# Optimization experiments

Measured on AMD Instinct MI355X. Metric: run time of the kernel, lower is better.

The kernel has to match this reference:

```python
import jax, jax.numpy as jnp
import numpy as np

EMBED_DIM = 1024
NUM_HEADS = 16
HEAD_DIM = EMBED_DIM // NUM_HEADS


def setup_inputs() -> dict:
    key = jax.random.key(0)
    ks = jax.random.split(key, 9)
    s = 1.0 / np.sqrt(EMBED_DIM)
    x = jax.random.normal(ks[0], (2, 2048, EMBED_DIM), dtype=jnp.float32)
    Wq = jax.random.uniform(ks[1], (EMBED_DIM, EMBED_DIM), jnp.float32, -s, s)
    bq = jax.random.uniform(ks[2], (EMBED_DIM,), jnp.float32, -s, s)
    Wk = jax.random.uniform(ks[3], (EMBED_DIM, EMBED_DIM), jnp.float32, -s, s)
    bk = jax.random.uniform(ks[4], (EMBED_DIM,), jnp.float32, -s, s)
    Wv = jax.random.uniform(ks[5], (EMBED_DIM, EMBED_DIM), jnp.float32, -s, s)
    bv = jax.random.uniform(ks[6], (EMBED_DIM,), jnp.float32, -s, s)
    Wo = jax.random.uniform(ks[7], (EMBED_DIM, EMBED_DIM), jnp.float32, -s, s)
    bo = jax.random.uniform(ks[8], (EMBED_DIM,), jnp.float32, -s, s)
    return {"x": x, "Wq": Wq, "bq": bq, "Wk": Wk, "bk": bk,
            "Wv": Wv, "bv": bv, "Wo": Wo, "bo": bo}


def reference(x, Wq, bq, Wk, bk, Wv, bv, Wo, bo):
    B, N, C = x.shape
    H, D = NUM_HEADS, HEAD_DIM
    # nn.Linear: y = x @ W.T + b; here W stored as [in, out] so y = x @ W + b
    def split_heads(y):
        return y.reshape(B, N, H, D).transpose(0, 2, 1, 3)  # [B,H,N,D]
    q = split_heads(x @ Wq + bq)
    k = split_heads(x @ Wk + bk)
    v = split_heads(x @ Wv + bv)
    scores = jnp.einsum('bhnd,bhmd->bhnm', q, k) / jnp.sqrt(jnp.float32(D)).astype(x.dtype)
    attn = jax.nn.softmax(scores, axis=-1)
    ctx = jnp.einsum('bhnm,bhmd->bhnd', attn, v)
    ctx = ctx.transpose(0, 2, 1, 3).reshape(B, N, C)
    return ctx @ Wo + bo
```

## Files before the change

kernel.cpp:

```cpp
#include <hip/hip_runtime.h>
#include <hip/hip_bf16.h>
#include <stdint.h>
#include <stddef.h>

using bf16 = __hip_bfloat16;
using bf16x8 = __attribute__((ext_vector_type(8))) short;
using f32x4  = __attribute__((ext_vector_type(4))) float;
using f32x16 = __attribute__((ext_vector_type(16))) float;
typedef unsigned int u32x2 __attribute__((ext_vector_type(2)));
typedef unsigned int u32x4 __attribute__((ext_vector_type(4)));

#define MFMA16(a, b, c) __builtin_amdgcn_mfma_f32_16x16x32_bf16((a), (b), (c), 0, 0, 0)
#define MFMA32(a, b, c) __builtin_amdgcn_mfma_f32_32x32x16_bf16((a), (b), (c), 0, 0, 0)

#define GLD16(g, l)                                                            \
  __builtin_amdgcn_global_load_lds(                                            \
      (const __attribute__((address_space(1))) void*)(g),                      \
      (__attribute__((address_space(3))) void*)(l), 16, 0, 0)

__device__ __forceinline__ float exp2_fast(float x) {
#if __has_builtin(__builtin_amdgcn_exp2f)
  return __builtin_amdgcn_exp2f(x);
#else
  return __expf(x * 0.69314718056f);
#endif
}

__device__ __forceinline__ float fmax3(float a, float b, float c) {
  return fmaxf(fmaxf(a, b), c);
}

__device__ __forceinline__ unsigned int cvtpk_bf16(float lo, float hi) {
  unsigned int r;
  asm("v_cvt_pk_bf16_f32 %0, %1, %2" : "=v"(r) : "v"(lo), "v"(hi));
  return r;
}

__device__ __forceinline__ void permswap(unsigned int& a, unsigned int& b, int hi) {
#if __has_builtin(__builtin_amdgcn_permlane32_swap)
  u32x2 r = __builtin_amdgcn_permlane32_swap(a, b, false, false);
  a = r.x;
  b = r.y;
#else
  unsigned int sa = __shfl_xor((unsigned int)a, 32, 64);
  unsigned int sb = __shfl_xor((unsigned int)b, 32, 64);
  unsigned int an = hi ? sb : a;
  unsigned int bn = hi ? b : sa;
  a = an; b = bn;
#endif
}


__global__ void convert_x(const float* __restrict__ x, bf16* __restrict__ out) {
  const int i = blockIdx.x * 256 + threadIdx.x;
  const float4 v = ((const float4*)x)[i];
  __hip_bfloat162* o2 = (__hip_bfloat162*)(out + (size_t)i * 4);
  o2[0] = __float22bfloat162_rn(make_float2(v.x, v.y));
  o2[1] = __float22bfloat162_rn(make_float2(v.z, v.w));
}

__global__ void convert_w(const float* __restrict__ W0, const float* __restrict__ W1,
                          const float* __restrict__ W2, const float* __restrict__ W3,
                          bf16* __restrict__ Wt) {
  __shared__ float t[32][33];
  const int bx = blockIdx.x;
  const int mat = bx >> 10;
  const float* W = (mat == 0) ? W0 : (mat == 1) ? W1 : (mat == 2) ? W2 : W3;
  const int rem = bx & 1023;
  const int k0 = (rem >> 5) * 32, n0 = (rem & 31) * 32;
  const int c = threadIdx.x & 31, r0 = (threadIdx.x >> 5) * 4;
#pragma unroll
  for (int i = 0; i < 4; ++i) {
    const int r = r0 + i;
    t[r][c] = W[(size_t)(k0 + r) * 1024 + n0 + c];
  }
  __syncthreads();
  bf16* dst = Wt + (size_t)mat * 1024 * 1024;
#pragma unroll
  for (int i = 0; i < 4; ++i) {
    const int rn = r0 + i;
    dst[(size_t)(n0 + rn) * 1024 + k0 + c] = __float2bfloat16(t[c][rn]);
  }
}

__global__ void concat_bias(const float* __restrict__ bq, const float* __restrict__ bk,
                            const float* __restrict__ bv, const float* __restrict__ bo,
                            float* __restrict__ dst) {
  const int i = blockIdx.x * 256 + threadIdx.x;
  const float* src = (i < 1024) ? bq : (i < 2048) ? bk : (i < 3072) ? bv : bo;
  dst[i] = src[i & 1023];
}


template <int MODE>
__global__ __launch_bounds__(256)
void gemm_bt(const bf16* __restrict__ A, const bf16* __restrict__ Bt,
             const float* __restrict__ bias,
             bf16* __restrict__ Qb, bf16* __restrict__ Kb, bf16* __restrict__ Vt,
             float* __restrict__ Of, int K) {
  __shared__ bf16 As[128 * 32];
  __shared__ bf16 Bs[128 * 32];
  const int tid = threadIdx.x;
  const int lane = tid & 63, w = tid >> 6;
  const int wr = w >> 1, wc = w & 1;
  const int lrow = lane & 15, lgk = lane >> 4;
  const int bm = blockIdx.y * 128, bn = blockIdx.x * 128;
  f32x4 acc[4][4] = {};
  const bf16* Ab = A + (size_t)bm * K;
  const bf16* Bb = Bt + (size_t)bn * K;
  const int e0 = tid, e1 = 256 + tid;

  for (int k0 = 0; k0 < K; k0 += 32) {
    GLD16(Ab + (size_t)(e0 >> 2) * K + k0 + (e0 & 3) * 8, As + e0 * 8);
    GLD16(Ab + (size_t)(e1 >> 2) * K + k0 + (e1 & 3) * 8, As + e1 * 8);
    GLD16(Bb + (size_t)(e0 >> 2) * K + k0 + (e0 & 3) * 8, Bs + e0 * 8);
    GLD16(Bb + (size_t)(e1 >> 2) * K + k0 + (e1 & 3) * 8, Bs + e1 * 8);
    asm volatile("s_waitcnt vmcnt(0)" ::: "memory");
    __syncthreads();
    bf16x8 af[4], bfr[4];
#pragma unroll
    for (int m = 0; m < 4; ++m)
      af[m] = *(const bf16x8*)(As + (wr * 64 + m * 16 + lrow) * 32 + lgk * 8);
#pragma unroll
    for (int n = 0; n < 4; ++n)
      bfr[n] = *(const bf16x8*)(Bs + (wc * 64 + n * 16 + lrow) * 32 + lgk * 8);
#pragma unroll
    for (int m = 0; m < 4; ++m)
#pragma unroll
      for (int n = 0; n < 4; ++n)
        acc[m][n] = MFMA16(af[m], bfr[n], acc[m][n]);
    __syncthreads();
  }

  if constexpr (MODE == 0) {
#pragma unroll
    for (int m = 0; m < 4; ++m) {
#pragma unroll
      for (int n = 0; n < 4; ++n) {
        const int col = bn + wc * 64 + n * 16 + lrow;
        const float bv_ = bias[col];
        const int row0 = bm + wr * 64 + m * 16 + lgk * 4;
        const int which = col >> 10;
        const int hd = col & 1023;
        const int h = hd >> 6, d = hd & 63;
        const int b = row0 >> 11, t0 = row0 & 2047;
        const int bh = b * 16 + h;
        if (which == 2) {
          uint2 pk;
          pk.x = cvtpk_bf16(acc[m][n][0] + bv_, acc[m][n][1] + bv_);
          pk.y = cvtpk_bf16(acc[m][n][2] + bv_, acc[m][n][3] + bv_);
          *(uint2*)(Vt + ((size_t)bh * 64 + d) * 2048 + t0) = pk;
        } else if (which == 0) {
#pragma unroll
          for (int j = 0; j < 4; ++j)
            Qb[((size_t)bh * 2048 + t0 + j) * 64 + d] =
                __float2bfloat16((acc[m][n][j] + bv_) * 0.18033688f);
        } else {
#pragma unroll
          for (int j = 0; j < 4; ++j)
            Kb[((size_t)bh * 2048 + t0 + j) * 64 + d] =
                __float2bfloat16(acc[m][n][j] + bv_);
        }
      }
    }
  } else {
#pragma unroll
    for (int m = 0; m < 4; ++m) {
#pragma unroll
      for (int n = 0; n < 4; ++n) {
        const int col = bn + wc * 64 + n * 16 + lrow;
        const float bv_ = bias[col];
        const int row0 = bm + wr * 64 + m * 16 + lgk * 4;
#pragma unroll
        for (int j = 0; j < 4; ++j)
          Of[(size_t)(row0 + j) * 1024 + col] = acc[m][n][j] + bv_;
      }
    }
  }
}

__global__ __launch_bounds__(256, 2)
void attn_kernel(const bf16* __restrict__ Q, const bf16* __restrict__ Kb,
                 const bf16* __restrict__ Vt, bf16* __restrict__ ctx) {
  __shared__ bf16 Kl[2][64 * 64];
  __shared__ bf16 Vl[2][64 * 64];

  const int tid = threadIdx.x, lane = tid & 63, w = tid >> 6;
  const int lo5 = lane & 31, hi = lane >> 5;

  const int bid = blockIdx.x;
  const int xcd = bid & 7, idx = bid >> 3;
  const int bh = (xcd << 2) | (idx >> 4);
  const int qt = idx & 15;
  const int q0 = qt * 128 + w * 32;

  const bf16* Qbh = Q + (size_t)bh * 2048 * 64;
  const bf16* Kbh = Kb + (size_t)bh * 2048 * 64;
  const bf16* Vbh = Vt + (size_t)bh * 64 * 2048;

  bf16x8 qf[4];
#pragma unroll
  for (int f = 0; f < 4; ++f)
    qf[f] = *(const bf16x8*)(Qbh + (size_t)(q0 + lo5) * 64 + f * 16 + hi * 8);

  f32x16 o0 = {}, o1 = {};
  float m2 = -1e30f;
  float lsum = 0.f;

  auto stage = [&](int buf, int kv) {
#pragma unroll
    for (int i = 0; i < 2; ++i) {
      const int c = (w * 2 + i) * 64 + lane;
      const int r = c >> 3, j = c & 7;
      const int js = (j ^ (r & 7)) * 8;
      GLD16(Kbh + (size_t)(kv + r) * 64 + js, &Kl[buf][c * 8]);
      GLD16(Vbh + (size_t)r * 2048 + kv + js, &Vl[buf][c * 8]);
    }
  };

  bf16x8 pa[4];

  auto softmax_pa = [&](f32x16& s0, f32x16& s1) {
    float r1[11];
#pragma unroll
    for (int i = 0; i < 5; ++i)
      r1[i] = fmax3(s0[3 * i], s0[3 * i + 1], s0[3 * i + 2]);
    r1[5] = fmax3(s0[15], s1[0], s1[1]);
#pragma unroll
    for (int i = 0; i < 4; ++i)
      r1[6 + i] = fmax3(s1[2 + 3 * i], s1[3 + 3 * i], s1[4 + 3 * i]);
    r1[10] = fmaxf(s1[14], s1[15]);
    float r2[4];
#pragma unroll
    for (int i = 0; i < 3; ++i) r2[i] = fmax3(r1[3 * i], r1[3 * i + 1], r1[3 * i + 2]);
    r2[3] = fmaxf(r1[9], r1[10]);
    const float pm = fmaxf(fmax3(r2[0], r2[1], r2[2]), r2[3]);
    if (!__all(pm <= m2 + 11.5416f)) {
      const float mx = fmaxf(pm, __shfl_xor(pm, 32, 64));
      const float mn = fmaxf(m2, mx);
      const float corr = exp2_fast(m2 - mn);
      m2 = mn;
      lsum *= corr;
#pragma unroll
      for (int j = 0; j < 16; ++j) { o0[j] *= corr; o1[j] *= corr; }
    }
#pragma unroll
    for (int j = 0; j < 16; ++j) s0[j] = exp2_fast(s0[j] - m2);
#pragma unroll
    for (int j = 0; j < 16; ++j) s1[j] = exp2_fast(s1[j] - m2);
    float a8[8];
#pragma unroll
    for (int j = 0; j < 8; ++j) a8[j] = (s0[j] + s0[j + 8]) + (s1[j] + s1[j + 8]);
    float a4[4];
#pragma unroll
    for (int j = 0; j < 4; ++j) a4[j] = a8[j] + a8[j + 4];
    lsum += (a4[0] + a4[1]) + (a4[2] + a4[3]);
#pragma unroll
    for (int ks = 0; ks < 4; ++ks) {
      const f32x16& s = (ks < 2) ? s0 : s1;
      const int b0 = (ks & 1) * 8;
      unsigned int a0 = cvtpk_bf16(s[b0 + 0], s[b0 + 1]);
      unsigned int c0 = cvtpk_bf16(s[b0 + 4], s[b0 + 5]);
      unsigned int a1 = cvtpk_bf16(s[b0 + 2], s[b0 + 3]);
      unsigned int c1 = cvtpk_bf16(s[b0 + 6], s[b0 + 7]);
      permswap(a0, c0, hi);
      permswap(a1, c1, hi);
      u32x4 tt;
      tt.x = a0; tt.y = a1; tt.z = c0; tt.w = c1;
      pa[ks] = __builtin_bit_cast(bf16x8, tt);
    }
  };

  f32x16 sA0, sA1, sB0, sB1;
  bf16x8 vfA[8], vfB[8];

  auto step = [&](int t, f32x16& sC0, f32x16& sC1, bf16x8 (&vfC)[8],
                  f32x16& sP0, f32x16& sP1, bf16x8 (&vfP)[8]) {
    const int cur = t & 1;
    const int kv = t << 6;
    if (t < 31) stage(cur ^ 1, kv + 64);
    if (t < 31)
      asm volatile("s_waitcnt vmcnt(4)" ::: "memory");
    else
      asm volatile("s_waitcnt vmcnt(0)" ::: "memory");
    __builtin_amdgcn_s_barrier();
    bf16x8 kf[8];
#pragma unroll
    for (int kt = 0; kt < 2; ++kt)
#pragma unroll
      for (int f = 0; f < 4; ++f) {
        const int r = kt * 32 + lo5;
        kf[kt * 4 + f] =
            *(const bf16x8*)(&Kl[cur][(r * 8 + (((f << 1) + hi) ^ (r & 7))) * 8]);
      }
#pragma unroll
    for (int dt = 0; dt < 2; ++dt)
#pragma unroll
      for (int ks = 0; ks < 4; ++ks) {
        const int r = dt * 32 + lo5;
        vfC[dt * 4 + ks] =
            *(const bf16x8*)(&Vl[cur][(r * 8 + (((ks << 1) + hi) ^ (r & 7))) * 8]);
      }
    if (t > 0) softmax_pa(sP0, sP1);
    asm volatile("s_waitcnt lgkmcnt(0)" ::: "memory");
    __builtin_amdgcn_sched_barrier(0);
    __builtin_amdgcn_s_barrier();
    __builtin_amdgcn_s_setprio(1);
    sC0 = f32x16{};
    sC1 = f32x16{};
#pragma unroll
    for (int f = 0; f < 4; ++f) sC0 = MFMA32(kf[f], qf[f], sC0);
#pragma unroll
    for (int f = 0; f < 4; ++f) sC1 = MFMA32(kf[4 + f], qf[f], sC1);
    if (t > 0) {
#pragma unroll
      for (int ks = 0; ks < 4; ++ks) {
        o0 = MFMA32(vfP[ks], pa[ks], o0);
        o1 = MFMA32(vfP[4 + ks], pa[ks], o1);
      }
    }
    __builtin_amdgcn_s_setprio(0);
  };

  stage(0, 0);

  step(0, sA0, sA1, vfA, sB0, sB1, vfB);
  for (int tt = 1; tt < 31; tt += 2) {
    step(tt, sB0, sB1, vfB, sA0, sA1, vfA);
    step(tt + 1, sA0, sA1, vfA, sB0, sB1, vfB);
  }
  step(31, sB0, sB1, vfB, sA0, sA1, vfA);

  softmax_pa(sB0, sB1);
#pragma unroll
  for (int ks = 0; ks < 4; ++ks) {
    o0 = MFMA32(vfB[ks], pa[ks], o0);
    o1 = MFMA32(vfB[4 + ks], pa[ks], o1);
  }

  lsum += __shfl_xor(lsum, 32, 64);
  const float inv = 1.f / lsum;
  const int b = bh >> 4, h = bh & 15;
  bf16* crow = ctx + (size_t)(b * 2048 + q0 + lo5) * 1024 + h * 64;
#pragma unroll
  for (int g = 0; g < 4; ++g) {
    uint2 pk0, pk1;
    pk0.x = cvtpk_bf16(o0[4 * g + 0] * inv, o0[4 * g + 1] * inv);
    pk0.y = cvtpk_bf16(o0[4 * g + 2] * inv, o0[4 * g + 3] * inv);
    pk1.x = cvtpk_bf16(o1[4 * g + 0] * inv, o1[4 * g + 1] * inv);
    pk1.y = cvtpk_bf16(o1[4 * g + 2] * inv, o1[4 * g + 3] * inv);
    *(uint2*)(crow + 8 * g + 4 * hi) = pk0;
    *(uint2*)(crow + 32 + 8 * g + 4 * hi) = pk1;
  }
}


extern "C" void kernel_launch(void* const* d_in, const int* in_sizes, int n_in,
                              void* d_out, int out_size, void* d_ws, size_t ws_size,
                              hipStream_t stream) {
  const float* x  = (const float*)d_in[0];
  const float* Wq = (const float*)d_in[1];
  const float* bq = (const float*)d_in[2];
  const float* Wk = (const float*)d_in[3];
  const float* bk = (const float*)d_in[4];
  const float* Wv = (const float*)d_in[5];
  const float* bv = (const float*)d_in[6];
  const float* Wo = (const float*)d_in[7];
  const float* bo = (const float*)d_in[8];
  float* out = (float*)d_out;

  char* ws = (char*)d_ws;
  bf16* xb  = (bf16*)(ws);
  bf16* Wt  = (bf16*)(ws + ((size_t)8 << 20));
  bf16* Qb  = (bf16*)(ws + ((size_t)16 << 20));
  bf16* Kb  = (bf16*)(ws + ((size_t)24 << 20));
  bf16* Vt  = (bf16*)(ws + ((size_t)32 << 20));
  bf16* ctx = (bf16*)(ws + ((size_t)40 << 20));
  float* ba = (float*)(ws + ((size_t)48 << 20));

  convert_x<<<dim3(4096), dim3(256), 0, stream>>>(x, xb);
  convert_w<<<dim3(4096), dim3(256), 0, stream>>>(Wq, Wk, Wv, Wo, Wt);
  concat_bias<<<dim3(16), dim3(256), 0, stream>>>(bq, bk, bv, bo, ba);

  gemm_bt<0><<<dim3(24, 32), dim3(256), 0, stream>>>(xb, Wt, ba, Qb, Kb, Vt, nullptr, 1024);

  attn_kernel<<<dim3(512), dim3(256), 0, stream>>>(Qb, Kb, Vt, ctx);

  gemm_bt<1><<<dim3(8, 32), dim3(256), 0, stream>>>(
      ctx, Wt + (size_t)3072 * 1024, ba + 3072, nullptr, nullptr, nullptr, out, 1024);
}
```

Baseline: 134.5 us.

## Triple-buffer GEMM and attention LDS loads, split output GEMM into narrower tiles

Both GEMMs now use a three-stage LDS ring with asynchronous global-to-LDS loads issued two tiles ahead, so loads overlap with MFMA work and each iteration needs one barrier instead of two. The attention kernel also moves to a three-deep K/V ring and drops its second barrier and LDS wait per step. The output projection uses 128x64 tiles, doubling the block count so more CUs are busy. In exchange LDS use per block rises, which may lower occupancy, and with fewer barriers there is a risk of overwrite races on the ring buffers.

After: 126.2 us. -6.2%, faster.

```diff
diff --git a/kernel.cpp b/kernel.cpp
--- a/kernel.cpp
+++ b/kernel.cpp
@@ -91,15 +91,13 @@
   dst[i] = src[i & 1023];
 }
 
-
-template <int MODE>
 __global__ __launch_bounds__(256)
-void gemm_bt(const bf16* __restrict__ A, const bf16* __restrict__ Bt,
-             const float* __restrict__ bias,
-             bf16* __restrict__ Qb, bf16* __restrict__ Kb, bf16* __restrict__ Vt,
-             float* __restrict__ Of, int K) {
-  __shared__ bf16 As[128 * 32];
-  __shared__ bf16 Bs[128 * 32];
+void gemm_qkv(const bf16* __restrict__ A, const bf16* __restrict__ Bt,
+              const float* __restrict__ bias,
+              bf16* __restrict__ Qb, bf16* __restrict__ Kb, bf16* __restrict__ Vt,
+              int K) {
+  __shared__ bf16 As[3][128 * 32];
+  __shared__ bf16 Bs[3][128 * 32];
   const int tid = threadIdx.x;
   const int lane = tid & 63, w = tid >> 6;
   const int wr = w >> 1, wc = w & 1;
@@ -109,72 +107,135 @@
   const bf16* Ab = A + (size_t)bm * K;
   const bf16* Bb = Bt + (size_t)bn * K;
   const int e0 = tid, e1 = 256 + tid;
-
-  for (int k0 = 0; k0 < K; k0 += 32) {
-    GLD16(Ab + (size_t)(e0 >> 2) * K + k0 + (e0 & 3) * 8, As + e0 * 8);
-    GLD16(Ab + (size_t)(e1 >> 2) * K + k0 + (e1 & 3) * 8, As + e1 * 8);
-    GLD16(Bb + (size_t)(e0 >> 2) * K + k0 + (e0 & 3) * 8, Bs + e0 * 8);
-    GLD16(Bb + (size_t)(e1 >> 2) * K + k0 + (e1 & 3) * 8, Bs + e1 * 8);
-    asm volatile("s_waitcnt vmcnt(0)" ::: "memory");
-    __syncthreads();
+  const int NT = K >> 5;
+
+  auto stage = [&](int s, int k0) {
+    GLD16(Ab + (size_t)(e0 >> 2) * K + k0 + (e0 & 3) * 8, &As[s][e0 * 8]);
+    GLD16(Ab + (size_t)(e1 >> 2) * K + k0 + (e1 & 3) * 8, &As[s][e1 * 8]);
+    GLD16(Bb + (size_t)(e0 >> 2) * K + k0 + (e0 & 3) * 8, &Bs[s][e0 * 8]);
+    GLD16(Bb + (size_t)(e1 >> 2) * K + k0 + (e1 & 3) * 8, &Bs[s][e1 * 8]);
+  };
+
+  stage(0, 0);
+  stage(1, 32);
+  int cur = 0, nxt = 2;
+  for (int t = 0; t < NT; ++t) {
+    if (t < NT - 1)
+      asm volatile("s_waitcnt vmcnt(4)" ::: "memory");
+    else
+      asm volatile("s_waitcnt vmcnt(0)" ::: "memory");
+    __builtin_amdgcn_s_barrier();
+    if (t + 2 < NT) {
+      stage(nxt, (t + 2) << 5);
+      nxt = (nxt == 2) ? 0 : nxt + 1;
+    }
     bf16x8 af[4], bfr[4];
 #pragma unroll
     for (int m = 0; m < 4; ++m)
-      af[m] = *(const bf16x8*)(As + (wr * 64 + m * 16 + lrow) * 32 + lgk * 8);
+      af[m] = *(const bf16x8*)(&As[cur][(wr * 64 + m * 16 + lrow) * 32 + lgk * 8]);
 #pragma unroll
     for (int n = 0; n < 4; ++n)
-      bfr[n] = *(const bf16x8*)(Bs + (wc * 64 + n * 16 + lrow) * 32 + lgk * 8);
+      bfr[n] = *(const bf16x8*)(&Bs[cur][(wc * 64 + n * 16 + lrow) * 32 + lgk * 8]);
 #pragma unroll
     for (int m = 0; m < 4; ++m)
 #pragma unroll
       for (int n = 0; n < 4; ++n)
         acc[m][n] = MFMA16(af[m], bfr[n], acc[m][n]);
-    __syncthreads();
-  }
-
-  if constexpr (MODE == 0) {
-#pragma unroll
-    for (int m = 0; m < 4; ++m) {
-#pragma unroll
-      for (int n = 0; n < 4; ++n) {
-        const int col = bn + wc * 64 + n * 16 + lrow;
-        const float bv_ = bias[col];
-        const int row0 = bm + wr * 64 + m * 16 + lgk * 4;
-        const int which = col >> 10;
-        const int hd = col & 1023;
-        const int h = hd >> 6, d = hd & 63;
-        const int b = row0 >> 11, t0 = row0 & 2047;
-        const int bh = b * 16 + h;
-        if (which == 2) {
-          uint2 pk;
-          pk.x = cvtpk_bf16(acc[m][n][0] + bv_, acc[m][n][1] + bv_);
-          pk.y = cvtpk_bf16(acc[m][n][2] + bv_, acc[m][n][3] + bv_);
-          *(uint2*)(Vt + ((size_t)bh * 64 + d) * 2048 + t0) = pk;
-        } else if (which == 0) {
-#pragma unroll
-          for (int j = 0; j < 4; ++j)
-            Qb[((size_t)bh * 2048 + t0 + j) * 64 + d] =
-                __float2bfloat16((acc[m][n][j] + bv_) * 0.18033688f);
-        } else {
-#pragma unroll
-          for (int j = 0; j < 4; ++j)
-            Kb[((size_t)bh * 2048 + t0 + j) * 64 + d] =
-                __float2bfloat16(acc[m][n][j] + bv_);
-        }
+    cur = (cur == 2) ? 0 : cur + 1;
+  }
+
+#pragma unroll
+  for (int m = 0; m < 4; ++m) {
+#pragma unroll
+    for (int n = 0; n < 4; ++n) {
+      const int col = bn + wc * 64 + n * 16 + lrow;
+      const float bv_ = bias[col];
+      const int row0 = bm + wr * 64 + m * 16 + lgk * 4;
+      const int which = col >> 10;
+      const int hd = col & 1023;
+      const int h = hd >> 6, d = hd & 63;
+      const int b = row0 >> 11, t0 = row0 & 2047;
+      const int bh = b * 16 + h;
+      if (which == 2) {
+        uint2 pk;
+        pk.x = cvtpk_bf16(acc[m][n][0] + bv_, acc[m][n][1] + bv_);
+        pk.y = cvtpk_bf16(acc[m][n][2] + bv_, acc[m][n][3] + bv_);
+        *(uint2*)(Vt + ((size_t)bh * 64 + d) * 2048 + t0) = pk;
+      } else if (which == 0) {
+#pragma unroll
+        for (int j = 0; j < 4; ++j)
+          Qb[((size_t)bh * 2048 + t0 + j) * 64 + d] =
+              __float2bfloat16((acc[m][n][j] + bv_) * 0.18033688f);
+      } else {
+#pragma unroll
+        for (int j = 0; j < 4; ++j)
+          Kb[((size_t)bh * 2048 + t0 + j) * 64 + d] =
+              __float2bfloat16(acc[m][n][j] + bv_);
       }
     }
-  } else {
-#pragma unroll
-    for (int m = 0; m < 4; ++m) {
-#pragma unroll
-      for (int n = 0; n < 4; ++n) {
-        const int col = bn + wc * 64 + n * 16 + lrow;
-        const float bv_ = bias[col];
-        const int row0 = bm + wr * 64 + m * 16 + lgk * 4;
-#pragma unroll
-        for (int j = 0; j < 4; ++j)
-          Of[(size_t)(row0 + j) * 1024 + col] = acc[m][n][j] + bv_;
-      }
+  }
+}
+
+__global__ __launch_bounds__(256)
+void gemm_o(const bf16* __restrict__ A, const bf16* __restrict__ Bt,
+            const float* __restrict__ bias, float* __restrict__ Of, int K) {
+  __shared__ bf16 As[3][128 * 32];
+  __shared__ bf16 Bs[3][64 * 32];
+  const int tid = threadIdx.x;
+  const int lane = tid & 63, w = tid >> 6;
+  const int wr = w >> 1, wc = w & 1;
+  const int lrow = lane & 15, lgk = lane >> 4;
+  const int bm = blockIdx.y * 128, bn = blockIdx.x * 64;
+  f32x4 acc[4][2] = {};
+  const bf16* Ab = A + (size_t)bm * K;
+  const bf16* Bb = Bt + (size_t)bn * K;
+  const int e0 = tid, e1 = 256 + tid;
+  const int NT = K >> 5;
+
+  auto stage = [&](int s, int k0) {
+    GLD16(Ab + (size_t)(e0 >> 2) * K + k0 + (e0 & 3) * 8, &As[s][e0 * 8]);
+    GLD16(Ab + (size_t)(e1 >> 2) * K + k0 + (e1 & 3) * 8, &As[s][e1 * 8]);
+    GLD16(Bb + (size_t)(e0 >> 2) * K + k0 + (e0 & 3) * 8, &Bs[s][e0 * 8]);
+  };
+
+  stage(0, 0);
+  stage(1, 32);
+  int cur = 0, nxt = 2;
+  for (int t = 0; t < NT; ++t) {
+    if (t < NT - 1)
+      asm volatile("s_waitcnt vmcnt(3)" ::: "memory");
+    else
+      asm volatile("s_waitcnt vmcnt(0)" ::: "memory");
+    __builtin_amdgcn_s_barrier();
+    if (t + 2 < NT) {
+      stage(nxt, (t + 2) << 5);
+      nxt = (nxt == 2) ? 0 : nxt + 1;
+    }
+    bf16x8 af[4], bfr[2];
+#pragma unroll
+    for (int m = 0; m < 4; ++m)
+      af[m] = *(const bf16x8*)(&As[cur][(wr * 64 + m * 16 + lrow) * 32 + lgk * 8]);
+#pragma unroll
+    for (int n = 0; n < 2; ++n)
+      bfr[n] = *(const bf16x8*)(&Bs[cur][(wc * 32 + n * 16 + lrow) * 32 + lgk * 8]);
+#pragma unroll
+    for (int m = 0; m < 4; ++m)
+#pragma unroll
+      for (int n = 0; n < 2; ++n)
+        acc[m][n] = MFMA16(af[m], bfr[n], acc[m][n]);
+    cur = (cur == 2) ? 0 : cur + 1;
+  }
+
+#pragma unroll
+  for (int m = 0; m < 4; ++m) {
+#pragma unroll
+    for (int n = 0; n < 2; ++n) {
+      const int col = bn + wc * 32 + n * 16 + lrow;
+      const float bv_ = bias[col];
+      const int row0 = bm + wr * 64 + m * 16 + lgk * 4;
+#pragma unroll
+      for (int j = 0; j < 4; ++j)
+        Of[(size_t)(row0 + j) * 1024 + col] = acc[m][n][j] + bv_;
     }
   }
 }
@@ -182,8 +243,8 @@
 __global__ __launch_bounds__(256, 2)
 void attn_kernel(const bf16* __restrict__ Q, const bf16* __restrict__ Kb,
                  const bf16* __restrict__ Vt, bf16* __restrict__ ctx) {
-  __shared__ bf16 Kl[2][64 * 64];
-  __shared__ bf16 Vl[2][64 * 64];
+  __shared__ bf16 Kl[3][64 * 64];
+  __shared__ bf16 Vl[3][64 * 64];
 
   const int tid = threadIdx.x, lane = tid & 63, w = tid >> 6;
   const int lo5 = lane & 31, hi = lane >> 5;
@@ -273,17 +334,20 @@
 
   f32x16 sA0, sA1, sB0, sB1;
   bf16x8 vfA[8], vfB[8];
+  int cur = 0, nxt = 2;
 
   auto step = [&](int t, f32x16& sC0, f32x16& sC1, bf16x8 (&vfC)[8],
                   f32x16& sP0, f32x16& sP1, bf16x8 (&vfP)[8]) {
-    const int cur = t & 1;
     const int kv = t << 6;
-    if (t < 31) stage(cur ^ 1, kv + 64);
     if (t < 31)
       asm volatile("s_waitcnt vmcnt(4)" ::: "memory");
     else
       asm volatile("s_waitcnt vmcnt(0)" ::: "memory");
     __builtin_amdgcn_s_barrier();
+    if (t + 2 < 32) {
+      stage(nxt, kv + 128);
+      nxt = (nxt == 2) ? 0 : nxt + 1;
+    }
     bf16x8 kf[8];
 #pragma unroll
     for (int kt = 0; kt < 2; ++kt)
@@ -302,9 +366,6 @@
             *(const bf16x8*)(&Vl[cur][(r * 8 + (((ks << 1) + hi) ^ (r & 7))) * 8]);
       }
     if (t > 0) softmax_pa(sP0, sP1);
-    asm volatile("s_waitcnt lgkmcnt(0)" ::: "memory");
-    __builtin_amdgcn_sched_barrier(0);
-    __builtin_amdgcn_s_barrier();
     __builtin_amdgcn_s_setprio(1);
     sC0 = f32x16{};
     sC1 = f32x16{};
@@ -320,9 +381,11 @@
       }
     }
     __builtin_amdgcn_s_setprio(0);
+    cur = (cur == 2) ? 0 : cur + 1;
   };
 
   stage(0, 0);
+  stage(1, 64);
 
   step(0, sA0, sA1, vfA, sB0, sB1, vfB);
   for (int tt = 1; tt < 31; tt += 2) {
@@ -382,10 +445,10 @@
   convert_w<<<dim3(4096), dim3(256), 0, stream>>>(Wq, Wk, Wv, Wo, Wt);
   concat_bias<<<dim3(16), dim3(256), 0, stream>>>(bq, bk, bv, bo, ba);
 
-  gemm_bt<0><<<dim3(24, 32), dim3(256), 0, stream>>>(xb, Wt, ba, Qb, Kb, Vt, nullptr, 1024);
+  gemm_qkv<<<dim3(24, 32), dim3(256), 0, stream>>>(xb, Wt, ba, Qb, Kb, Vt, 1024);
 
   attn_kernel<<<dim3(512), dim3(256), 0, stream>>>(Qb, Kb, Vt, ctx);
 
-  gemm_bt<1><<<dim3(8, 32), dim3(256), 0, stream>>>(
-      ctx, Wt + (size_t)3072 * 1024, ba + 3072, nullptr, nullptr, nullptr, out, 1024);
-}
+  gemm_o<<<dim3(16, 32), dim3(256), 0, stream>>>(
+      ctx, Wt + (size_t)3072 * 1024, ba + 3072, out, 1024);
+}
```
